# Optimization experiments

Hardware: AMD Instinct MI355X
Metric: run time of the kernel (lower is better)

Reference implementation:

```python
import jax, jax.numpy as jnp
import numpy as np

N = 50000
D = 256
E = 800000


def setup_inputs() -> dict:
    key = jax.random.key(0)
    ks = jax.random.split(key, 9)
    X = jax.random.normal(ks[0], (N, D), dtype=jnp.float32)
    edge_index = jax.random.randint(ks[1], (2, E), 0, N, dtype=jnp.int32)
    edge_weight = jax.random.uniform(ks[2], (E,), dtype=jnp.float32)
    p = jax.random.normal(ks[3], (D,), dtype=jnp.float32)
    s = 1.0 / np.sqrt(D)
    W_ih = jax.random.normal(ks[4], (3 * D, D), dtype=jnp.float32) * s
    W_hh = jax.random.normal(ks[5], (3 * D, D), dtype=jnp.float32) * s
    b_ih = jax.random.normal(ks[6], (3 * D,), dtype=jnp.float32) * s
    b_hh = jax.random.normal(ks[7], (3 * D,), dtype=jnp.float32) * s
    W0 = jax.random.normal(ks[8], (D, D), dtype=jnp.float32) * s
    return {"X": X, "edge_index": edge_index, "edge_weight": edge_weight,
            "p": p, "W_ih": W_ih, "W_hh": W_hh, "b_ih": b_ih, "b_hh": b_hh, "W0": W0}


def reference(X, edge_index, edge_weight, p, W_ih, W_hh, b_ih, b_hh, W0):
    n, d = X.shape  # n=N, d=D; ratio = d/n -> TopK keeps k=d nodes
    k = d

    # ---- TopKPooling: score = X.p/||p||, keep top-k, gate by tanh(score) ----
    score = X @ p / jnp.linalg.norm(p)          # [n]
    top_score, idx = jax.lax.top_k(score, k)    # [k]
    x_tilde = X[idx] * jnp.tanh(top_score)[:, None]  # [k, d]

    # ---- Single-step GRU: input x_tilde (batch=k=d), hidden = conv weight W0 [d,d] ----
    h = W0
    gi = x_tilde @ W_ih.T + b_ih                # [d, 3d]
    gh = h @ W_hh.T + b_hh                      # [d, 3d]
    i_r, i_z, i_n = jnp.split(gi, 3, axis=1)
    h_r, h_z, h_n = jnp.split(gh, 3, axis=1)
    r = jax.nn.sigmoid(i_r + h_r)
    z = jax.nn.sigmoid(i_z + h_z)
    nn_ = jnp.tanh(i_n + r * h_n)
    W_new = (1.0 - z) * nn_ + z * h             # evolved conv weight [d, d]

    # ---- GCNConv (no bias): x = X @ W, symmetric norm with self-loops ----
    xw = X @ W_new                              # [n, d]
    src, dst = edge_index[0], edge_index[1]
    loop = jnp.arange(n, dtype=src.dtype)
    src_f = jnp.concatenate([src, loop])
    dst_f = jnp.concatenate([dst, loop])
    ew_f = jnp.concatenate([edge_weight, jnp.ones((n,), dtype=X.dtype)])
    deg = jax.ops.segment_sum(ew_f, dst_f, num_segments=n)  # [n]
    dinv = jnp.where(deg > 0, jax.lax.rsqrt(deg), 0.0)
    norm = dinv[src_f] * ew_f * dinv[dst_f]     # [E+n]
    msgs = norm[:, None] * xw[src_f]            # [E+n, d] gather
    out = jax.ops.segment_sum(msgs, dst_f, num_segments=n)  # scatter-add
    return out
```

## Files before the change

### kernel.cpp

```cpp
#include <hip/hip_runtime.h>
#include <cstdint>
#include <cstddef>

#define N_NODES 50000
#define DIM     256
#define NEDGE   800000
#define TOPK    256
#define HBINS   65536
#define CAND_CAP 2048
#define SLOT    64

typedef unsigned long long u64;
typedef float f32x4 __attribute__((ext_vector_type(4)));
typedef __bf16 b16x8 __attribute__((ext_vector_type(8)));
typedef unsigned short us8 __attribute__((ext_vector_type(8)));

__device__ __forceinline__ u64 okey(double d) {
  u64 b = (u64)__double_as_longlong(d);
  return (b & 0x8000000000000000ULL) ? ~b : (b | 0x8000000000000000ULL);
}

__device__ __forceinline__ unsigned short f2bf(float f) {
  unsigned u = __float_as_uint(f);
  return (unsigned short)((u + 0x7fffu + ((u >> 16) & 1u)) >> 16);
}

__device__ __forceinline__ float bf2f(unsigned short u) {
  return __uint_as_float(((unsigned)u) << 16);
}

__global__ void pnorm_kernel(const float* __restrict__ p, double* __restrict__ pn) {
  __shared__ double red[256];
  int t = threadIdx.x;
  double v = (double)p[t];
  red[t] = v * v;
  __syncthreads();
  for (int off = 128; off > 0; off >>= 1) {
    if (t < off) red[t] += red[t + off];
    __syncthreads();
  }
  if (t == 0) *pn = sqrt(red[0]);
}

__global__ __launch_bounds__(256) void score_kernel(const float* __restrict__ X,
                             const float* __restrict__ p,
                             double* __restrict__ scores, unsigned* __restrict__ hist) {
  int lane = threadIdx.x & 63;
  int gw = blockIdx.x * 4 + (threadIdx.x >> 6);
  int nw = gridDim.x * 4;
  float4 p4 = reinterpret_cast<const float4*>(p)[lane];
  for (int row = gw; row < N_NODES; row += nw) {
    float4 x4 = reinterpret_cast<const float4*>(X + (size_t)row * DIM)[lane];
    double s = (double)x4.x * p4.x + (double)x4.y * p4.y +
               (double)x4.z * p4.z + (double)x4.w * p4.w;
    for (int off = 32; off > 0; off >>= 1) s += __shfl_xor(s, off, 64);
    if (lane == 0) {
      scores[row] = s;
      unsigned bin = (unsigned)(okey(s) >> 48);
      atomicAdd(&hist[bin], 1u);
    }
  }
}

__global__ __launch_bounds__(1024) void findbin_kernel(const unsigned* __restrict__ hist,
                                                       int* __restrict__ ctrl) {
  __shared__ int sums[1024];
  int t = threadIdx.x;
  int base = t * 64;
  const uint4* h4 = reinterpret_cast<const uint4*>(hist + base);
  int s = 0;
#pragma unroll
  for (int i = 0; i < 16; ++i) {
    uint4 v = h4[i];
    s += (int)(v.x + v.y + v.z + v.w);
  }
  sums[t] = s;
  __syncthreads();
  for (int off = 1; off < 1024; off <<= 1) {
    int x = (t + off < 1024) ? sums[t + off] : 0;
    __syncthreads();
    sums[t] += x;
    __syncthreads();
  }
  int S_incl = sums[t];
  int S_excl = S_incl - s;
  if (S_excl < TOPK && S_incl >= TOPK) {
    int c = S_excl;
    int thr = base;
    for (int b = base + 63; b >= base; --b) {
      c += (int)hist[b];
      if (c >= TOPK) { thr = b; break; }
    }
    ctrl[0] = thr;
  }
}

__global__ void collect_kernel(const double* __restrict__ scores, int* __restrict__ ctrl,
                               double* __restrict__ cand_s, int* __restrict__ cand_i) {
  int i = blockIdx.x * 256 + threadIdx.x;
  if (i >= N_NODES) return;
  double sc = scores[i];
  int bin = (int)(okey(sc) >> 48);
  if (bin >= ctrl[0]) {
    int pos = atomicAdd(&ctrl[1], 1);
    if (pos < CAND_CAP) { cand_s[pos] = sc; cand_i[pos] = i; }
  }
}

__global__ __launch_bounds__(1024) void sort_kernel(const int* __restrict__ ctrl,
                                                    const double* __restrict__ cand_s,
                                                    const int* __restrict__ cand_i,
                                                    const double* __restrict__ pn,
                                                    int* __restrict__ top_idx,
                                                    float* __restrict__ gate) {
  __shared__ double cs[CAND_CAP];
  __shared__ int ci[CAND_CAP];
  int t = threadIdx.x;
  int cnt = ctrl[1];
  if (cnt > CAND_CAP) cnt = CAND_CAP;
  for (int s = 0; s < CAND_CAP / 1024; ++s) {
    int i = t + s * 1024;
    if (i < cnt) { cs[i] = cand_s[i]; ci[i] = cand_i[i]; }
    else         { cs[i] = -1e308;    ci[i] = 0x7fffffff; }
  }
  __syncthreads();
  for (int k2 = 2; k2 <= CAND_CAP; k2 <<= 1) {
    for (int j = k2 >> 1; j > 0; j >>= 1) {
      for (int s = 0; s < CAND_CAP / 1024; ++s) {
        int i = t + s * 1024;
        int ixj = i ^ j;
        if (ixj > i) {
          double si = cs[i], sx = cs[ixj];
          int ii = ci[i], ix = ci[ixj];
          bool up = ((i & k2) == 0);
          bool sw = up ? ((sx > si) || (sx == si && ix < ii))
                       : ((si > sx) || (si == sx && ii < ix));
          if (sw) { cs[i] = sx; cs[ixj] = si; ci[i] = ix; ci[ixj] = ii; }
        }
      }
      __syncthreads();
    }
  }
  if (t < TOPK) {
    top_idx[t] = ci[t];
    gate[t] = (float)tanh(cs[t] / *pn);
  }
}

__global__ void xtilde_kernel(const float* __restrict__ X, const int* __restrict__ top_idx,
                              const float* __restrict__ gate, float* __restrict__ xt) {
  int r = blockIdx.x;
  int lane = threadIdx.x;
  float g = gate[r];
  int src = top_idx[r];
  float4 v = reinterpret_cast<const float4*>(X + (size_t)src * DIM)[lane];
  v.x *= g; v.y *= g; v.z *= g; v.w *= g;
  reinterpret_cast<float4*>(xt + (size_t)r * DIM)[lane] = v;
}

__global__ __launch_bounds__(256) void gru_gemm_kernel(const float* __restrict__ xt,
                                const float* __restrict__ W0,
                                const float* __restrict__ W_ih, const float* __restrict__ W_hh,
                                const float* __restrict__ b_ih, const float* __restrict__ b_hh,
                                float* __restrict__ gi, float* __restrict__ gh) {
  __shared__ float As[8][DIM];
  int tid = threadIdx.x;
  int c = blockIdx.x * 256 + tid;
  int r0 = blockIdx.y * 8;
  int which = blockIdx.z;
  const float* A = which ? W0 : xt;
  const float* W = which ? W_hh : W_ih;
  const float* b = which ? b_hh : b_ih;
  float* outp = which ? gh : gi;
  {
    const float4* src = reinterpret_cast<const float4*>(A + (size_t)r0 * DIM);
    float4* dst = reinterpret_cast<float4*>(&As[0][0]);
    dst[tid] = src[tid];
    dst[tid + 256] = src[tid + 256];
  }
  __syncthreads();
  const float4* Wr = reinterpret_cast<const float4*>(W + (size_t)c * DIM);
  float acc[8] = {0, 0, 0, 0, 0, 0, 0, 0};
#pragma unroll 4
  for (int k4 = 0; k4 < DIM / 4; ++k4) {
    float4 w = Wr[k4];
#pragma unroll
    for (int r = 0; r < 8; ++r) {
      acc[r] += As[r][k4 * 4 + 0] * w.x + As[r][k4 * 4 + 1] * w.y +
                As[r][k4 * 4 + 2] * w.z + As[r][k4 * 4 + 3] * w.w;
    }
  }
  float bc = b[c];
#pragma unroll
  for (int r = 0; r < 8; ++r)
    outp[(size_t)(r0 + r) * 768 + c] = acc[r] + bc;
}

__global__ void wnew_kernel(const float* __restrict__ gi, const float* __restrict__ gh,
                            const float* __restrict__ W0, unsigned short* __restrict__ Wnbt) {
  int rr = blockIdx.x, c = threadIdx.x;
  const float* gir = gi + (size_t)rr * 768;
  const float* ghr = gh + (size_t)rr * 768;
  float i_r = gir[c],       h_r = ghr[c];
  float i_z = gir[c + 256], h_z = ghr[c + 256];
  float i_n = gir[c + 512], h_n = ghr[c + 512];
  float r = 1.f / (1.f + expf(-(i_r + h_r)));
  float z = 1.f / (1.f + expf(-(i_z + h_z)));
  float nn = tanhf(i_n + r * h_n);
  float h = W0[(size_t)rr * DIM + c];
  float w = (1.f - z) * nn + z * h;
  Wnbt[(size_t)c * DIM + rr] = f2bf(w);
}

__global__ __launch_bounds__(256) void xw_mfma_kernel(const float* __restrict__ X,
                                                      const unsigned short* __restrict__ Wnbt,
                                                      unsigned short* __restrict__ xwb) {
  int wid = threadIdx.x >> 6, lane = threadIdx.x & 63;
  int r0 = blockIdx.x * 64 + wid * 16;
  if (r0 >= N_NODES) return;
  int rowA = r0 + (lane & 15);
  int kgrp = lane >> 4;
  int koff = kgrp * 8;

  const float4* Ar = reinterpret_cast<const float4*>(X + (size_t)rowA * DIM);
  b16x8 afr[8];
#pragma unroll
  for (int kt = 0; kt < 8; ++kt) {
    float4 f0 = Ar[kt * 8 + kgrp * 2 + 0];
    float4 f1 = Ar[kt * 8 + kgrp * 2 + 1];
    union { us8 u; b16x8 b; } cv;
    cv.u[0] = f2bf(f0.x); cv.u[1] = f2bf(f0.y); cv.u[2] = f2bf(f0.z); cv.u[3] = f2bf(f0.w);
    cv.u[4] = f2bf(f1.x); cv.u[5] = f2bf(f1.y); cv.u[6] = f2bf(f1.z); cv.u[7] = f2bf(f1.w);
    afr[kt] = cv.b;
  }

  int colB = lane & 15;
  const unsigned short* Bbase = Wnbt + (size_t)colB * DIM + koff;
  int rr = r0 + kgrp * 4;
#pragma unroll 4
  for (int nf = 0; nf < 16; ++nf) {
    f32x4 acc = {0.f, 0.f, 0.f, 0.f};
    const unsigned short* Bp = Bbase + (size_t)nf * 16 * DIM;
#pragma unroll
    for (int kt = 0; kt < 8; ++kt) {
      b16x8 bfr = *reinterpret_cast<const b16x8*>(Bp + kt * 32);
      acc = __builtin_amdgcn_mfma_f32_16x16x32_bf16(afr[kt], bfr, acc, 0, 0, 0);
    }
    int cc = nf * 16 + colB;
#pragma unroll
    for (int j = 0; j < 4; ++j)
      xwb[(size_t)(rr + j) * DIM + cc] = f2bf(acc[j]);
  }
}

__global__ __launch_bounds__(256) void scatter_kernel(const int* __restrict__ ei,
                               const float* __restrict__ ew,
                               float* __restrict__ deg,
                               int* __restrict__ fill, u64* __restrict__ colval) {
  int stride = gridDim.x * 256;
  for (int e = blockIdx.x * 256 + threadIdx.x; e < NEDGE; e += stride) {
    int s = ei[e], d = ei[NEDGE + e];
    float w = ew[e];
    atomicAdd(&deg[d], w);
    int pos = atomicAdd(&fill[d], 1);
    if (pos < SLOT)
      colval[(size_t)d * SLOT + pos] = ((u64)__float_as_uint(w) << 32) | (unsigned)s;
  }
}

__global__ void dinv_kernel(const float* __restrict__ deg, float* __restrict__ dinvb) {
  int i = blockIdx.x * 256 + threadIdx.x;
  if (i >= N_NODES) return;
  dinvb[i] = __frsqrt_rn(deg[i] + 1.0f);
}

__global__ __launch_bounds__(256) void agg_kernel(const unsigned short* __restrict__ xwb,
                           const float* __restrict__ dinvb,
                           const int* __restrict__ fill, const u64* __restrict__ colval,
                           float* __restrict__ out) {
  int lane = threadIdx.x & 63;
  int gw = blockIdx.x * 4 + (threadIdx.x >> 6);
  int nw = gridDim.x * 4;
  for (int i = gw; i < N_NODES; i += nw) {
    float di = dinvb[i];
    ushort4 sv = reinterpret_cast<const ushort4*>(xwb + (size_t)i * DIM)[lane];
    float4 acc;
    acc.x = di * bf2f(sv.x); acc.y = di * bf2f(sv.y);
    acc.z = di * bf2f(sv.z); acc.w = di * bf2f(sv.w);
    int n = fill[i];
    if (n > SLOT) n = SLOT;
    const u64* cv = colval + (size_t)i * SLOT;
    int j = 0;
    for (; j + 4 <= n; j += 4) {
      u64 a0 = cv[j], a1 = cv[j + 1], a2 = cv[j + 2], a3 = cv[j + 3];
      unsigned c0 = (unsigned)a0, c1 = (unsigned)a1, c2 = (unsigned)a2, c3 = (unsigned)a3;
      ushort4 m0 = reinterpret_cast<const ushort4*>(xwb + (size_t)c0 * DIM)[lane];
      ushort4 m1 = reinterpret_cast<const ushort4*>(xwb + (size_t)c1 * DIM)[lane];
      ushort4 m2 = reinterpret_cast<const ushort4*>(xwb + (size_t)c2 * DIM)[lane];
      ushort4 m3 = reinterpret_cast<const ushort4*>(xwb + (size_t)c3 * DIM)[lane];
      float v0 = __uint_as_float((unsigned)(a0 >> 32)) * dinvb[c0];
      float v1 = __uint_as_float((unsigned)(a1 >> 32)) * dinvb[c1];
      float v2 = __uint_as_float((unsigned)(a2 >> 32)) * dinvb[c2];
      float v3 = __uint_as_float((unsigned)(a3 >> 32)) * dinvb[c3];
      acc.x += v0 * bf2f(m0.x); acc.y += v0 * bf2f(m0.y);
      acc.z += v0 * bf2f(m0.z); acc.w += v0 * bf2f(m0.w);
      acc.x += v1 * bf2f(m1.x); acc.y += v1 * bf2f(m1.y);
      acc.z += v1 * bf2f(m1.z); acc.w += v1 * bf2f(m1.w);
      acc.x += v2 * bf2f(m2.x); acc.y += v2 * bf2f(m2.y);
      acc.z += v2 * bf2f(m2.z); acc.w += v2 * bf2f(m2.w);
      acc.x += v3 * bf2f(m3.x); acc.y += v3 * bf2f(m3.y);
      acc.z += v3 * bf2f(m3.z); acc.w += v3 * bf2f(m3.w);
    }
    for (; j < n; ++j) {
      u64 a0 = cv[j];
      unsigned c0 = (unsigned)a0;
      ushort4 m0 = reinterpret_cast<const ushort4*>(xwb + (size_t)c0 * DIM)[lane];
      float v0 = __uint_as_float((unsigned)(a0 >> 32)) * dinvb[c0];
      acc.x += v0 * bf2f(m0.x); acc.y += v0 * bf2f(m0.y);
      acc.z += v0 * bf2f(m0.z); acc.w += v0 * bf2f(m0.w);
    }
    acc.x *= di; acc.y *= di; acc.z *= di; acc.w *= di;
    reinterpret_cast<float4*>(out + (size_t)i * DIM)[lane] = acc;
  }
}

extern "C" void kernel_launch(void* const* d_in, const int* in_sizes, int n_in,
                              void* d_out, int out_size, void* d_ws, size_t ws_size,
                              hipStream_t stream) {
  const float* X    = (const float*)d_in[0];
  const int*   ei   = (const int*)d_in[1];
  const float* ew   = (const float*)d_in[2];
  const float* p    = (const float*)d_in[3];
  const float* W_ih = (const float*)d_in[4];
  const float* W_hh = (const float*)d_in[5];
  const float* b_ih = (const float*)d_in[6];
  const float* b_hh = (const float*)d_in[7];
  const float* W0   = (const float*)d_in[8];
  float* out = (float*)d_out;

  char* ws = (char*)d_ws;
  size_t off = 0;
  auto alloc = [&](size_t bytes) { size_t o = off; off = (off + bytes + 255) & ~(size_t)255; return o; };

  size_t hist_o  = alloc(HBINS * 4);
  size_t ctrl_o  = alloc(64);
  size_t deg_o   = alloc(N_NODES * 4);
  size_t fill_o  = alloc(N_NODES * 4);
  size_t zero_span = off;
  size_t scores_o = alloc(N_NODES * 8);
  size_t pn_o     = alloc(8);
  size_t cands_o  = alloc(CAND_CAP * 8);
  size_t candi_o  = alloc(CAND_CAP * 4);
  size_t topidx_o = alloc(TOPK * 4);
  size_t gate_o   = alloc(TOPK * 4);
  size_t dinv_o   = alloc(N_NODES * 4);
  size_t xt_o     = alloc((size_t)TOPK * DIM * 4);
  size_t gi_o     = alloc((size_t)256 * 768 * 4);
  size_t gh_o     = alloc((size_t)256 * 768 * 4);
  size_t wnbt_o   = alloc((size_t)DIM * DIM * 2);
  size_t colval_o = alloc((size_t)N_NODES * SLOT * 8);
  size_t xwb_o    = alloc((size_t)N_NODES * DIM * 2);
  (void)ws_size; (void)n_in; (void)in_sizes; (void)out_size;

  unsigned* hist  = (unsigned*)(ws + hist_o);
  int*    ctrl    = (int*)(ws + ctrl_o);
  float*  deg     = (float*)(ws + deg_o);
  int*    fill    = (int*)(ws + fill_o);
  double* scores  = (double*)(ws + scores_o);
  double* pn      = (double*)(ws + pn_o);
  double* cand_s  = (double*)(ws + cands_o);
  int*    cand_i  = (int*)(ws + candi_o);
  int*    top_idx = (int*)(ws + topidx_o);
  float*  gate    = (float*)(ws + gate_o);
  float*  dinvb   = (float*)(ws + dinv_o);
  float*  xt      = (float*)(ws + xt_o);
  float*  gi      = (float*)(ws + gi_o);
  float*  gh      = (float*)(ws + gh_o);
  unsigned short* Wnbt = (unsigned short*)(ws + wnbt_o);
  u64*    colval  = (u64*)(ws + colval_o);
  unsigned short* xwb = (unsigned short*)(ws + xwb_o);

  hipMemsetAsync(ws, 0, zero_span, stream);

  pnorm_kernel<<<1, 256, 0, stream>>>(p, pn);
  score_kernel<<<1024, 256, 0, stream>>>(X, p, scores, hist);
  findbin_kernel<<<1, 1024, 0, stream>>>(hist, ctrl);
  collect_kernel<<<(N_NODES + 255) / 256, 256, 0, stream>>>(scores, ctrl, cand_s, cand_i);
  sort_kernel<<<1, 1024, 0, stream>>>(ctrl, cand_s, cand_i, pn, top_idx, gate);
  xtilde_kernel<<<TOPK, 64, 0, stream>>>(X, top_idx, gate, xt);
  gru_gemm_kernel<<<dim3(3, 32, 2), 256, 0, stream>>>(xt, W0, W_ih, W_hh, b_ih, b_hh, gi, gh);
  wnew_kernel<<<256, 256, 0, stream>>>(gi, gh, W0, Wnbt);
  xw_mfma_kernel<<<(N_NODES + 63) / 64, 256, 0, stream>>>(X, Wnbt, xwb);
  scatter_kernel<<<1024, 256, 0, stream>>>(ei, ew, deg, fill, colval);
  dinv_kernel<<<(N_NODES + 255) / 256, 256, 0, stream>>>(deg, dinvb);
  agg_kernel<<<2048, 256, 0, stream>>>(xwb, dinvb, fill, colval, out);
}
```

Before: 529.5 us.

## Fuse small kernels into neighbors and unroll score and aggregation loops

```diff
diff --git a/kernel.cpp b/kernel.cpp
--- a/kernel.cpp
+++ b/kernel.cpp
@@ -29,19 +29,6 @@
   return __uint_as_float(((unsigned)u) << 16);
 }
 
-__global__ void pnorm_kernel(const float* __restrict__ p, double* __restrict__ pn) {
-  __shared__ double red[256];
-  int t = threadIdx.x;
-  double v = (double)p[t];
-  red[t] = v * v;
-  __syncthreads();
-  for (int off = 128; off > 0; off >>= 1) {
-    if (t < off) red[t] += red[t + off];
-    __syncthreads();
-  }
-  if (t == 0) *pn = sqrt(red[0]);
-}
-
 __global__ __launch_bounds__(256) void score_kernel(const float* __restrict__ X,
                              const float* __restrict__ p,
                              double* __restrict__ scores, unsigned* __restrict__ hist) {
@@ -49,7 +36,31 @@
   int gw = blockIdx.x * 4 + (threadIdx.x >> 6);
   int nw = gridDim.x * 4;
   float4 p4 = reinterpret_cast<const float4*>(p)[lane];
-  for (int row = gw; row < N_NODES; row += nw) {
+  int row = gw;
+  for (; row + 7 * nw < N_NODES; row += 8 * nw) {
+    float4 x[8];
+#pragma unroll
+    for (int u = 0; u < 8; ++u)
+      x[u] = reinterpret_cast<const float4*>(X + (size_t)(row + u * nw) * DIM)[lane];
+    double s[8];
+#pragma unroll
+    for (int u = 0; u < 8; ++u)
+      s[u] = (double)x[u].x * p4.x + (double)x[u].y * p4.y +
+             (double)x[u].z * p4.z + (double)x[u].w * p4.w;
+    for (int off = 32; off > 0; off >>= 1) {
+#pragma unroll
+      for (int u = 0; u < 8; ++u) s[u] += __shfl_xor(s[u], off, 64);
+    }
+    if (lane == 0) {
+#pragma unroll
+      for (int u = 0; u < 8; ++u) {
+        scores[row + u * nw] = s[u];
+        unsigned bin = (unsigned)(okey(s[u]) >> 48);
+        atomicAdd(&hist[bin], 1u);
+      }
+    }
+  }
+  for (; row < N_NODES; row += nw) {
     float4 x4 = reinterpret_cast<const float4*>(X + (size_t)row * DIM)[lane];
     double s = (double)x4.x * p4.x + (double)x4.y * p4.y +
                (double)x4.z * p4.z + (double)x4.w * p4.w;
@@ -110,23 +121,40 @@
 __global__ __launch_bounds__(1024) void sort_kernel(const int* __restrict__ ctrl,
                                                     const double* __restrict__ cand_s,
                                                     const int* __restrict__ cand_i,
-                                                    const double* __restrict__ pn,
+                                                    const float* __restrict__ p,
                                                     int* __restrict__ top_idx,
                                                     float* __restrict__ gate) {
   __shared__ double cs[CAND_CAP];
   __shared__ int ci[CAND_CAP];
+  __shared__ double pred[256];
   int t = threadIdx.x;
+  if (t < 256) {
+    double v = (double)p[t];
+    pred[t] = v * v;
+  }
   int cnt = ctrl[1];
   if (cnt > CAND_CAP) cnt = CAND_CAP;
-  for (int s = 0; s < CAND_CAP / 1024; ++s) {
+  int M = (cnt <= 1024) ? 1024 : CAND_CAP;
+  for (int s = 0; s < M / 1024; ++s) {
     int i = t + s * 1024;
     if (i < cnt) { cs[i] = cand_s[i]; ci[i] = cand_i[i]; }
     else         { cs[i] = -1e308;    ci[i] = 0x7fffffff; }
   }
   __syncthreads();
-  for (int k2 = 2; k2 <= CAND_CAP; k2 <<= 1) {
+  if (t < 128) pred[t] += pred[t + 128];
+  __syncthreads();
+  if (t < 64) pred[t] += pred[t + 64];
+  __syncthreads();
+  if (t < 32) { pred[t] += pred[t + 32]; }
+  __syncthreads();
+  if (t == 0) {
+    double acc = 0.0;
+    for (int i = 0; i < 32; ++i) acc += pred[i];
+    pred[0] = sqrt(acc);
+  }
+  for (int k2 = 2; k2 <= M; k2 <<= 1) {
     for (int j = k2 >> 1; j > 0; j >>= 1) {
-      for (int s = 0; s < CAND_CAP / 1024; ++s) {
+      for (int s = 0; s < M / 1024; ++s) {
         int i = t + s * 1024;
         int ixj = i ^ j;
         if (ixj > i) {
@@ -143,22 +171,12 @@
   }
   if (t < TOPK) {
     top_idx[t] = ci[t];
-    gate[t] = (float)tanh(cs[t] / *pn);
-  }
-}
-
-__global__ void xtilde_kernel(const float* __restrict__ X, const int* __restrict__ top_idx,
-                              const float* __restrict__ gate, float* __restrict__ xt) {
-  int r = blockIdx.x;
-  int lane = threadIdx.x;
-  float g = gate[r];
-  int src = top_idx[r];
-  float4 v = reinterpret_cast<const float4*>(X + (size_t)src * DIM)[lane];
-  v.x *= g; v.y *= g; v.z *= g; v.w *= g;
-  reinterpret_cast<float4*>(xt + (size_t)r * DIM)[lane] = v;
-}
-
-__global__ __launch_bounds__(256) void gru_gemm_kernel(const float* __restrict__ xt,
+    gate[t] = (float)tanh(cs[t] / pred[0]);
+  }
+}
+
+__global__ __launch_bounds__(256) void gru_gemm_kernel(const float* __restrict__ X,
+                                const int* __restrict__ top_idx, const float* __restrict__ gate,
                                 const float* __restrict__ W0,
                                 const float* __restrict__ W_ih, const float* __restrict__ W_hh,
                                 const float* __restrict__ b_ih, const float* __restrict__ b_hh,
@@ -168,15 +186,26 @@
   int c = blockIdx.x * 256 + tid;
   int r0 = blockIdx.y * 8;
   int which = blockIdx.z;
-  const float* A = which ? W0 : xt;
   const float* W = which ? W_hh : W_ih;
   const float* b = which ? b_hh : b_ih;
   float* outp = which ? gh : gi;
-  {
-    const float4* src = reinterpret_cast<const float4*>(A + (size_t)r0 * DIM);
+  if (which) {
+    const float4* src = reinterpret_cast<const float4*>(W0 + (size_t)r0 * DIM);
     float4* dst = reinterpret_cast<float4*>(&As[0][0]);
     dst[tid] = src[tid];
     dst[tid + 256] = src[tid + 256];
+  } else {
+#pragma unroll
+    for (int h = 0; h < 2; ++h) {
+      int idx2 = tid + h * 256;
+      int r = idx2 >> 6;
+      int e = idx2 & 63;
+      int srcrow = top_idx[r0 + r];
+      float g = gate[r0 + r];
+      float4 v = reinterpret_cast<const float4*>(X + (size_t)srcrow * DIM)[e];
+      v.x *= g; v.y *= g; v.z *= g; v.w *= g;
+      reinterpret_cast<float4*>(&As[0][0])[idx2] = v;
+    }
   }
   __syncthreads();
   const float4* Wr = reinterpret_cast<const float4*>(W + (size_t)c * DIM);
@@ -268,21 +297,15 @@
   }
 }
 
-__global__ void dinv_kernel(const float* __restrict__ deg, float* __restrict__ dinvb) {
-  int i = blockIdx.x * 256 + threadIdx.x;
-  if (i >= N_NODES) return;
-  dinvb[i] = __frsqrt_rn(deg[i] + 1.0f);
-}
-
 __global__ __launch_bounds__(256) void agg_kernel(const unsigned short* __restrict__ xwb,
-                           const float* __restrict__ dinvb,
+                           const float* __restrict__ deg,
                            const int* __restrict__ fill, const u64* __restrict__ colval,
                            float* __restrict__ out) {
   int lane = threadIdx.x & 63;
   int gw = blockIdx.x * 4 + (threadIdx.x >> 6);
   int nw = gridDim.x * 4;
   for (int i = gw; i < N_NODES; i += nw) {
-    float di = dinvb[i];
+    float di = __frsqrt_rn(deg[i] + 1.0f);
     ushort4 sv = reinterpret_cast<const ushort4*>(xwb + (size_t)i * DIM)[lane];
     float4 acc;
     acc.x = di * bf2f(sv.x); acc.y = di * bf2f(sv.y);
@@ -291,31 +314,31 @@
     if (n > SLOT) n = SLOT;
     const u64* cv = colval + (size_t)i * SLOT;
     int j = 0;
-    for (; j + 4 <= n; j += 4) {
-      u64 a0 = cv[j], a1 = cv[j + 1], a2 = cv[j + 2], a3 = cv[j + 3];
-      unsigned c0 = (unsigned)a0, c1 = (unsigned)a1, c2 = (unsigned)a2, c3 = (unsigned)a3;
-      ushort4 m0 = reinterpret_cast<const ushort4*>(xwb + (size_t)c0 * DIM)[lane];
-      ushort4 m1 = reinterpret_cast<const ushort4*>(xwb + (size_t)c1 * DIM)[lane];
-      ushort4 m2 = reinterpret_cast<const ushort4*>(xwb + (size_t)c2 * DIM)[lane];
-      ushort4 m3 = reinterpret_cast<const ushort4*>(xwb + (size_t)c3 * DIM)[lane];
-      float v0 = __uint_as_float((unsigned)(a0 >> 32)) * dinvb[c0];
-      float v1 = __uint_as_float((unsigned)(a1 >> 32)) * dinvb[c1];
-      float v2 = __uint_as_float((unsigned)(a2 >> 32)) * dinvb[c2];
-      float v3 = __uint_as_float((unsigned)(a3 >> 32)) * dinvb[c3];
-      acc.x += v0 * bf2f(m0.x); acc.y += v0 * bf2f(m0.y);
-      acc.z += v0 * bf2f(m0.z); acc.w += v0 * bf2f(m0.w);
-      acc.x += v1 * bf2f(m1.x); acc.y += v1 * bf2f(m1.y);
-      acc.z += v1 * bf2f(m1.z); acc.w += v1 * bf2f(m1.w);
-      acc.x += v2 * bf2f(m2.x); acc.y += v2 * bf2f(m2.y);
-      acc.z += v2 * bf2f(m2.z); acc.w += v2 * bf2f(m2.w);
-      acc.x += v3 * bf2f(m3.x); acc.y += v3 * bf2f(m3.y);
-      acc.z += v3 * bf2f(m3.z); acc.w += v3 * bf2f(m3.w);
+    for (; j + 8 <= n; j += 8) {
+      u64 a[8];
+#pragma unroll
+      for (int u = 0; u < 8; ++u) a[u] = cv[j + u];
+      unsigned c[8];
+      ushort4 m[8];
+      float dg[8];
+#pragma unroll
+      for (int u = 0; u < 8; ++u) {
+        c[u] = (unsigned)a[u];
+        m[u] = reinterpret_cast<const ushort4*>(xwb + (size_t)c[u] * DIM)[lane];
+        dg[u] = deg[c[u]];
+      }
+#pragma unroll
+      for (int u = 0; u < 8; ++u) {
+        float v = __uint_as_float((unsigned)(a[u] >> 32)) * __frsqrt_rn(dg[u] + 1.0f);
+        acc.x += v * bf2f(m[u].x); acc.y += v * bf2f(m[u].y);
+        acc.z += v * bf2f(m[u].z); acc.w += v * bf2f(m[u].w);
+      }
     }
     for (; j < n; ++j) {
       u64 a0 = cv[j];
       unsigned c0 = (unsigned)a0;
       ushort4 m0 = reinterpret_cast<const ushort4*>(xwb + (size_t)c0 * DIM)[lane];
-      float v0 = __uint_as_float((unsigned)(a0 >> 32)) * dinvb[c0];
+      float v0 = __uint_as_float((unsigned)(a0 >> 32)) * __frsqrt_rn(deg[c0] + 1.0f);
       acc.x += v0 * bf2f(m0.x); acc.y += v0 * bf2f(m0.y);
       acc.z += v0 * bf2f(m0.z); acc.w += v0 * bf2f(m0.w);
     }
@@ -348,13 +371,10 @@
   size_t fill_o  = alloc(N_NODES * 4);
   size_t zero_span = off;
   size_t scores_o = alloc(N_NODES * 8);
-  size_t pn_o     = alloc(8);
   size_t cands_o  = alloc(CAND_CAP * 8);
   size_t candi_o  = alloc(CAND_CAP * 4);
   size_t topidx_o = alloc(TOPK * 4);
   size_t gate_o   = alloc(TOPK * 4);
-  size_t dinv_o   = alloc(N_NODES * 4);
-  size_t xt_o     = alloc((size_t)TOPK * DIM * 4);
   size_t gi_o     = alloc((size_t)256 * 768 * 4);
   size_t gh_o     = alloc((size_t)256 * 768 * 4);
   size_t wnbt_o   = alloc((size_t)DIM * DIM * 2);
@@ -367,13 +387,10 @@
   float*  deg     = (float*)(ws + deg_o);
   int*    fill    = (int*)(ws + fill_o);
   double* scores  = (double*)(ws + scores_o);
-  double* pn      = (double*)(ws + pn_o);
   double* cand_s  = (double*)(ws + cands_o);
   int*    cand_i  = (int*)(ws + candi_o);
   int*    top_idx = (int*)(ws + topidx_o);
   float*  gate    = (float*)(ws + gate_o);
-  float*  dinvb   = (float*)(ws + dinv_o);
-  float*  xt      = (float*)(ws + xt_o);
   float*  gi      = (float*)(ws + gi_o);
   float*  gh      = (float*)(ws + gh_o);
   unsigned short* Wnbt = (unsigned short*)(ws + wnbt_o);
@@ -382,16 +399,14 @@
 
   hipMemsetAsync(ws, 0, zero_span, stream);
 
-  pnorm_kernel<<<1, 256, 0, stream>>>(p, pn);
-  score_kernel<<<1024, 256, 0, stream>>>(X, p, scores, hist);
+  score_kernel<<<1563, 256, 0, stream>>>(X, p, scores, hist);
   findbin_kernel<<<1, 1024, 0, stream>>>(hist, ctrl);
   collect_kernel<<<(N_NODES + 255) / 256, 256, 0, stream>>>(scores, ctrl, cand_s, cand_i);
-  sort_kernel<<<1, 1024, 0, stream>>>(ctrl, cand_s, cand_i, pn, top_idx, gate);
-  xtilde_kernel<<<TOPK, 64, 0, stream>>>(X, top_idx, gate, xt);
-  gru_gemm_kernel<<<dim3(3, 32, 2), 256, 0, stream>>>(xt, W0, W_ih, W_hh, b_ih, b_hh, gi, gh);
+  sort_kernel<<<1, 1024, 0, stream>>>(ctrl, cand_s, cand_i, p, top_idx, gate);
+  gru_gemm_kernel<<<dim3(3, 32, 2), 256, 0, stream>>>(X, top_idx, gate, W0, W_ih, W_hh,
+                                                      b_ih, b_hh, gi, gh);
   wnew_kernel<<<256, 256, 0, stream>>>(gi, gh, W0, Wnbt);
   xw_mfma_kernel<<<(N_NODES + 63) / 64, 256, 0, stream>>>(X, Wnbt, xwb);
   scatter_kernel<<<1024, 256, 0, stream>>>(ei, ew, deg, fill, colval);
-  dinv_kernel<<<(N_NODES + 255) / 256, 256, 0, stream>>>(deg, dinvb);
-  agg_kernel<<<2048, 256, 0, stream>>>(xwb, dinvb, fill, colval, out);
-}
+  agg_kernel<<<2048, 256, 0, stream>>>(xwb, deg, fill, colval, out);
+}
```

After: 494.1 us. 1.07x faster.
